# Optimization experiments

Measured on AMD Instinct MI355X. Metric: run time of the kernel, lower is better.

## Reference

```python
import jax, jax.numpy as jnp
import numpy as np

NMS_RADIUS = 0.05  # matches init_kwargs nms_radius


def setup_inputs() -> dict:
    key = jax.random.key(0)
    heatmap = jax.random.normal(key, (64, 1, 1024, 1024), dtype=jnp.float32)
    return {"heatmap": heatmap, "num_candidates": 16}


def _nms_select(coords, num_keep, radius):
    """Greedy sequential 2D NMS over score-sorted coords [k,2].
    torch.topk already returns values sorted descending, so the torch
    argsort(descending=True) is the identity permutation here."""
    k = coords.shape[0]
    # pairwise euclidean distances [k,k]
    d = jnp.linalg.norm(coords[:, None, :] - coords[None, :, :], axis=-1)

    def body(carry, i):
        mask, count = carry  # mask[j] = candidate j already selected
        too_close = jnp.any((d[i] < radius) & mask)
        accept = jnp.logical_and(~too_close, count < num_keep)
        mask = mask.at[i].set(accept)
        count = count + accept.astype(jnp.int32)
        return (mask, count), None

    (mask, _), _ = jax.lax.scan(body, (jnp.zeros(k, bool), jnp.int32(0)), jnp.arange(k))
    # compact: place selected coords (in score order) into the first num_keep slots
    pos = jnp.cumsum(mask) - 1               # output slot for each selected candidate
    slot = jnp.where(mask, pos, num_keep)    # out-of-range slot for unselected -> dropped
    out = jnp.zeros((num_keep, 2), coords.dtype).at[slot].set(coords, mode="drop")
    return out


def reference(heatmap, num_candidates):
    B, _, H, W = heatmap.shape
    flat = heatmap.reshape(B, H * W)
    k = min(num_candidates * 4, H * W)
    top_vals, top_idx = jax.lax.top_k(flat, k)   # sorted descending, like torch.topk
    ty = top_idx // W
    tx = top_idx % W
    # normalized (x, y) in [0,1], shape [B, k, 2]
    coords = jnp.stack([tx.astype(jnp.float32) / (W - 1),
                        ty.astype(jnp.float32) / (H - 1)], axis=-1)
    return jax.vmap(lambda c: _nms_select(c, num_candidates, NMS_RADIUS))(coords)
```

## Files before the change

### kernel.cpp

```cpp
#include <hip/hip_runtime.h>
#include <float.h>
#include <limits.h>

#define RADIUS 0.05f
#define TH     3.0f
#define LCAP   1024
#define SORTN  2048

typedef unsigned long long u64;

__device__ __forceinline__ unsigned fkey(float f) {
  unsigned u = __float_as_uint(f);
  return (u & 0x80000000u) ? ~u : (u | 0x80000000u);
}

__global__ __launch_bounds__(256) void zero_k(unsigned* cnt, int* bad, int B) {
  int t = blockIdx.x * blockDim.x + threadIdx.x;
  if (t < B * 16) cnt[t] = 0u;
  if (t < B) bad[t] = 0;
}

__global__ __launch_bounds__(256) void scan_collect(
    const float* __restrict__ hm, unsigned* __restrict__ cnt, int* __restrict__ bad,
    u64* __restrict__ buf, int bcap, int elems, int chunk) {
  const int b   = blockIdx.y;
  const int tid = threadIdx.x;
  const int vbase = blockIdx.x * chunk;
  const float4* p = (const float4*)(hm + (size_t)b * elems) + vbase;

  __shared__ u64 sbuf[LCAP];
  __shared__ unsigned sh, sbase;
  if (tid == 0) sh = 0u;
  __syncthreads();

  auto push = [&](float v, int idx) {
    if (v > TH) {
      unsigned pos = atomicAdd(&sh, 1u);
      if (pos < LCAP)
        sbuf[pos] = ((u64)(__float_as_uint(v) | 0x80000000u) << 32) | (unsigned)(~idx);
    }
  };

  int chunkMain = chunk & ~1023;
  for (int i = tid; i < chunkMain; i += 1024) {
    float4 v0 = p[i], v1 = p[i + 256], v2 = p[i + 512], v3 = p[i + 768];
    int g0 = (vbase + i) << 2, g1 = (vbase + i + 256) << 2;
    int g2 = (vbase + i + 512) << 2, g3 = (vbase + i + 768) << 2;
    push(v0.x, g0); push(v0.y, g0 + 1); push(v0.z, g0 + 2); push(v0.w, g0 + 3);
    push(v1.x, g1); push(v1.y, g1 + 1); push(v1.z, g1 + 2); push(v1.w, g1 + 3);
    push(v2.x, g2); push(v2.y, g2 + 1); push(v2.z, g2 + 2); push(v2.w, g2 + 3);
    push(v3.x, g3); push(v3.y, g3 + 1); push(v3.z, g3 + 2); push(v3.w, g3 + 3);
  }
  for (int i = chunkMain + tid; i < chunk; i += 256) {
    float4 v = p[i];
    int g = (vbase + i) << 2;
    push(v.x, g); push(v.y, g + 1); push(v.z, g + 2); push(v.w, g + 3);
  }

  __syncthreads();
  unsigned h = sh;
  unsigned stored = h < (unsigned)LCAP ? h : (unsigned)LCAP;
  if (tid == 0) {
    sbase = atomicAdd(&cnt[b * 16], stored);
    if (h > (unsigned)LCAP || sbase + stored > (unsigned)bcap) atomicExch(&bad[b], 1);
  }
  __syncthreads();
  unsigned gb = sbase;
  for (unsigned i = tid; i < stored; i += 256) {
    unsigned dst = gb + i;
    if (dst < (unsigned)bcap) buf[(size_t)b * bcap + dst] = sbuf[i];
  }
}

__global__ __launch_bounds__(256) void select_k(
    const float* __restrict__ hm, const unsigned* __restrict__ cnt,
    const int* __restrict__ bad, const u64* __restrict__ buf, int bcap,
    float* __restrict__ out, int W, int H, int K, int nk, int elems) {
  const int b = blockIdx.x, tid = threadIdx.x;

  __shared__ u64 s[SORTN];
  __shared__ unsigned s_cnt;
  __shared__ int s_m;
  __shared__ float topx[64], topy[64];
  __shared__ float outbuf[128];

  int c = 0;
  bool good = false;
  if (bcap > 0) {
    c = (int)cnt[b * 16];
    good = (!bad[b]) && (c >= K) && (c <= bcap) && (c <= SORTN);
  }

  if (good) {
    for (int i = tid; i < SORTN; i += 256)
      s[i] = (i < c) ? buf[(size_t)b * bcap + i] : 0ull;
  } else {
    unsigned lo = 0u, hi = 0xFFFFFFFFu;
    const float4* p4 = (const float4*)(hm + (size_t)b * elems);
    const int nvec4 = elems >> 2;
    while (lo < hi) {
      unsigned mid = lo + ((hi - lo) >> 1) + 1u;
      if (tid == 0) s_cnt = 0u;
      __syncthreads();
      unsigned local = 0;
      for (int i = tid; i < nvec4; i += 256) {
        float4 v = p4[i];
        local += (fkey(v.x) >= mid) + (fkey(v.y) >= mid) + (fkey(v.z) >= mid) + (fkey(v.w) >= mid);
      }
      atomicAdd(&s_cnt, local);
      __syncthreads();
      if (s_cnt >= (unsigned)K) lo = mid; else hi = mid - 1u;
      __syncthreads();
    }
    if (tid == 0) s_m = 0;
    __syncthreads();
    const float* q = hm + (size_t)b * elems;
    for (int i = tid; i < elems; i += 256) {
      unsigned kk = fkey(q[i]);
      if (kk >= lo) {
        int pos = atomicAdd(&s_m, 1);
        if (pos < SORTN) s[pos] = ((u64)kk << 32) | (unsigned)(~i);
      }
    }
    __syncthreads();
    int c2 = s_m < SORTN ? s_m : SORTN;
    for (int i = tid; i < SORTN; i += 256)
      if (i >= c2) s[i] = 0ull;
  }
  __syncthreads();

  for (int k2 = 2; k2 <= SORTN; k2 <<= 1) {
    for (int j = k2 >> 1; j > 0; j >>= 1) {
      for (int i = tid; i < SORTN; i += 256) {
        int ix = i ^ j;
        if (ix > i) {
          u64 a = s[i], bb = s[ix];
          bool desc = ((i & k2) == 0);
          bool sw = desc ? (a < bb) : (a > bb);
          if (sw) { s[i] = bb; s[ix] = a; }
        }
      }
      __syncthreads();
    }
  }

  const float invW = 1.0f / (float)(W - 1);
  const float invH = 1.0f / (float)(H - 1);
  if (tid < K) {
    u64 e = s[tid];
    int idx = (int)(~(unsigned)(e & 0xFFFFFFFFu));
    int ty = idx / W;
    int tx = idx - ty * W;
    topx[tid] = (float)tx * invW;
    topy[tid] = (float)ty * invH;
  }
  for (int i = tid; i < 2 * nk; i += 256) outbuf[i] = 0.0f;
  __syncthreads();

  if (tid < 64) {
    float myx = (tid < K) ? topx[tid] : 0.0f;
    float myy = (tid < K) ? topy[tid] : 0.0f;
    bool sel = false;
    int cntA = 0;
    for (int i = 0; i < K; i++) {
      float xi = __shfl(myx, i);
      float yi = __shfl(myy, i);
      float dx = myx - xi, dy = myy - yi;
      bool close = sel && (sqrtf(dx * dx + dy * dy) < RADIUS);
      u64 anym = __ballot(close);
      bool accept = (anym == 0ull) && (cntA < nk);
      if (tid == i) sel = accept;
      cntA += accept ? 1 : 0;
    }
    u64 selball = __ballot(sel);
    if (sel) {
      int slot = __popcll(selball & ((1ull << tid) - 1ull));
      if (slot < nk) { outbuf[2 * slot] = myx; outbuf[2 * slot + 1] = myy; }
    }
  }
  __syncthreads();

  float* outp = out + (size_t)b * 2 * nk;
  for (int i = tid; i < 2 * nk; i += 256) outp[i] = outbuf[i];
}

extern "C" void kernel_launch(void* const* d_in, const int* in_sizes, int n_in,
                              void* d_out, int out_size, void* d_ws, size_t ws_size,
                              hipStream_t stream) {
  const float* hm = (const float*)d_in[0];
  const int H = 1024, W = 1024;
  const int elems = H * W;
  int B = in_sizes[0] / elems;
  int nk = out_size / (B * 2);
  int K = 4 * nk;
  if (K > elems) K = elems;
  if (K > 64) K = 64;

  unsigned* cnt = (unsigned*)d_ws;
  size_t off_bad = (size_t)B * 16 * sizeof(unsigned);
  int* bad = (int*)((char*)d_ws + off_bad);
  size_t off_buf = (off_bad + (size_t)B * sizeof(int) + 255) & ~(size_t)255;
  u64* buf = (u64*)((char*)d_ws + off_buf);
  int bcap = 0;
  if (ws_size > off_buf) {
    size_t avail = ws_size - off_buf;
    long long capl = (long long)(avail / ((size_t)B * sizeof(u64)));
    bcap = (capl > SORTN) ? SORTN : (int)capl;
  }

  zero_k<<<(B * 16 + 255) / 256, 256, 0, stream>>>(cnt, bad, B);
  if (bcap > 0) {
    const int gx = 16;
    int chunk = (elems >> 2) / gx;
    dim3 grid(gx, B);
    scan_collect<<<grid, 256, 0, stream>>>(hm, cnt, bad, buf, bcap, elems, chunk);
  }
  select_k<<<B, 256, 0, stream>>>(hm, cnt, bad, buf, bcap, (float*)d_out, W, H, K, nk, elems);
}
```

Baseline: 440.3 us.

## Replace full 2048-element bitonic sort with radix-select threshold and small top sort

Each scan block now writes its candidates to a private per-block segment with its own count, which removes the zero kernel, the global atomic counter and the bad flag. The select kernel concatenates the segments, binary-searches a key threshold over the candidates in shared memory to isolate the top K, and then bitonic-sorts only 128 entries instead of 2048. Wave-level shuffle reductions replace per-thread shared atomics in the counting loops. This cuts the sorting work and one kernel launch, but the per-block buffer shrinks to 256 entries, so overflow forces the slow full-heatmap fallback more often.

```diff
diff --git a/kernel.cpp b/kernel.cpp
--- a/kernel.cpp
+++ b/kernel.cpp
@@ -1,11 +1,10 @@
 #include <hip/hip_runtime.h>
-#include <float.h>
-#include <limits.h>
 
 #define RADIUS 0.05f
 #define TH     3.0f
-#define LCAP   1024
+#define SBUF   256
 #define SORTN  2048
+#define TOPC   128
 
 typedef unsigned long long u64;
 
@@ -14,29 +13,24 @@
   return (u & 0x80000000u) ? ~u : (u | 0x80000000u);
 }
 
-__global__ __launch_bounds__(256) void zero_k(unsigned* cnt, int* bad, int B) {
-  int t = blockIdx.x * blockDim.x + threadIdx.x;
-  if (t < B * 16) cnt[t] = 0u;
-  if (t < B) bad[t] = 0;
-}
-
 __global__ __launch_bounds__(256) void scan_collect(
-    const float* __restrict__ hm, unsigned* __restrict__ cnt, int* __restrict__ bad,
-    u64* __restrict__ buf, int bcap, int elems, int chunk) {
+    const float* __restrict__ hm, unsigned* __restrict__ cnt,
+    u64* __restrict__ buf, int bcapblk, int elems, int chunk) {
   const int b   = blockIdx.y;
+  const int g   = blockIdx.x;
   const int tid = threadIdx.x;
-  const int vbase = blockIdx.x * chunk;
+  const int vbase = g * chunk;
   const float4* p = (const float4*)(hm + (size_t)b * elems) + vbase;
 
-  __shared__ u64 sbuf[LCAP];
-  __shared__ unsigned sh, sbase;
+  __shared__ u64 sbuf[SBUF];
+  __shared__ unsigned sh;
   if (tid == 0) sh = 0u;
   __syncthreads();
 
   auto push = [&](float v, int idx) {
     if (v > TH) {
       unsigned pos = atomicAdd(&sh, 1u);
-      if (pos < LCAP)
+      if (pos < SBUF)
         sbuf[pos] = ((u64)(__float_as_uint(v) | 0x80000000u) << 32) | (unsigned)(~idx);
     }
   };
@@ -53,47 +47,87 @@
   }
   for (int i = chunkMain + tid; i < chunk; i += 256) {
     float4 v = p[i];
-    int g = (vbase + i) << 2;
-    push(v.x, g); push(v.y, g + 1); push(v.z, g + 2); push(v.w, g + 3);
+    int gg = (vbase + i) << 2;
+    push(v.x, gg); push(v.y, gg + 1); push(v.z, gg + 2); push(v.w, gg + 3);
   }
 
   __syncthreads();
   unsigned h = sh;
-  unsigned stored = h < (unsigned)LCAP ? h : (unsigned)LCAP;
-  if (tid == 0) {
-    sbase = atomicAdd(&cnt[b * 16], stored);
-    if (h > (unsigned)LCAP || sbase + stored > (unsigned)bcap) atomicExch(&bad[b], 1);
-  }
-  __syncthreads();
-  unsigned gb = sbase;
-  for (unsigned i = tid; i < stored; i += 256) {
-    unsigned dst = gb + i;
-    if (dst < (unsigned)bcap) buf[(size_t)b * bcap + dst] = sbuf[i];
-  }
+  unsigned cap = (unsigned)bcapblk; if (cap > (unsigned)SBUF) cap = SBUF;
+  unsigned stored = h < cap ? h : cap;
+  u64* dst = buf + (size_t)(b * 16 + g) * (size_t)bcapblk;
+  for (unsigned i = tid; i < stored; i += 256) dst[i] = sbuf[i];
+  if (tid == 0)
+    cnt[b * 16 + g] = stored | (h > stored ? 0x80000000u : 0u);
 }
 
 __global__ __launch_bounds__(256) void select_k(
     const float* __restrict__ hm, const unsigned* __restrict__ cnt,
-    const int* __restrict__ bad, const u64* __restrict__ buf, int bcap,
+    const u64* __restrict__ buf, int bcapblk,
     float* __restrict__ out, int W, int H, int K, int nk, int elems) {
   const int b = blockIdx.x, tid = threadIdx.x;
 
   __shared__ u64 s[SORTN];
+  __shared__ unsigned skey[SORTN];
+  __shared__ u64 top[TOPC];
+  __shared__ unsigned segoff[17];
+  __shared__ int s_good, s_m;
   __shared__ unsigned s_cnt;
-  __shared__ int s_m;
   __shared__ float topx[64], topy[64];
   __shared__ float outbuf[128];
 
-  int c = 0;
-  bool good = false;
-  if (bcap > 0) {
-    c = (int)cnt[b * 16];
-    good = (!bad[b]) && (c >= K) && (c <= bcap) && (c <= SORTN);
-  }
+  if (tid == 0) {
+    unsigned tot = 0; int ok = (bcapblk > 0);
+    for (int g = 0; g < 16; g++) {
+      unsigned cv = (bcapblk > 0) ? cnt[b * 16 + g] : 0u;
+      segoff[g] = tot;
+      if (cv & 0x80000000u) ok = 0;
+      tot += (cv & 0x7FFFFFFFu);
+    }
+    segoff[16] = tot;
+    s_good = ok && tot >= (unsigned)K && tot <= (unsigned)SORTN;
+    s_m = 0;
+  }
+  __syncthreads();
+  const int good = s_good;
+  const unsigned c = segoff[16];
 
   if (good) {
-    for (int i = tid; i < SORTN; i += 256)
-      s[i] = (i < c) ? buf[(size_t)b * bcap + i] : 0ull;
+    for (int g = 0; g < 16; g++) {
+      unsigned off = segoff[g], len = segoff[g + 1] - off;
+      const u64* src = buf + (size_t)(b * 16 + g) * (size_t)bcapblk;
+      for (unsigned i = tid; i < len; i += 256) {
+        u64 e = src[i];
+        s[off + i] = e;
+        skey[off + i] = (unsigned)(e >> 32);
+      }
+    }
+    __syncthreads();
+
+    unsigned lo = 0xC0400000u;
+    unsigned hi = 0xFFFFFFFFu;
+    while (lo < hi) {
+      unsigned mid = lo + ((hi - lo) >> 1) + 1u;
+      if (tid == 0) s_cnt = 0u;
+      __syncthreads();
+      unsigned local = 0;
+      for (unsigned i = tid; i < c; i += 256) local += (skey[i] >= mid);
+      #pragma unroll
+      for (int o = 32; o > 0; o >>= 1) local += __shfl_xor(local, o);
+      if ((tid & 63) == 0) atomicAdd(&s_cnt, local);
+      __syncthreads();
+      unsigned tot = s_cnt;
+      if (tot >= (unsigned)K) lo = mid; else hi = mid - 1u;
+      __syncthreads();
+    }
+
+    for (unsigned i = tid; i < c; i += 256) {
+      if (skey[i] >= lo) {
+        int p = atomicAdd(&s_m, 1);
+        if (p < TOPC) top[p] = s[i];
+      }
+    }
+    __syncthreads();
   } else {
     unsigned lo = 0u, hi = 0xFFFFFFFFu;
     const float4* p4 = (const float4*)(hm + (size_t)b * elems);
@@ -107,37 +141,35 @@
         float4 v = p4[i];
         local += (fkey(v.x) >= mid) + (fkey(v.y) >= mid) + (fkey(v.z) >= mid) + (fkey(v.w) >= mid);
       }
-      atomicAdd(&s_cnt, local);
+      #pragma unroll
+      for (int o = 32; o > 0; o >>= 1) local += __shfl_xor(local, o);
+      if ((tid & 63) == 0) atomicAdd(&s_cnt, local);
       __syncthreads();
       if (s_cnt >= (unsigned)K) lo = mid; else hi = mid - 1u;
       __syncthreads();
     }
-    if (tid == 0) s_m = 0;
-    __syncthreads();
     const float* q = hm + (size_t)b * elems;
     for (int i = tid; i < elems; i += 256) {
       unsigned kk = fkey(q[i]);
       if (kk >= lo) {
-        int pos = atomicAdd(&s_m, 1);
-        if (pos < SORTN) s[pos] = ((u64)kk << 32) | (unsigned)(~i);
+        int p = atomicAdd(&s_m, 1);
+        if (p < TOPC) top[p] = ((u64)kk << 32) | (unsigned)(~i);
       }
     }
     __syncthreads();
-    int c2 = s_m < SORTN ? s_m : SORTN;
-    for (int i = tid; i < SORTN; i += 256)
-      if (i >= c2) s[i] = 0ull;
-  }
-  __syncthreads();
-
-  for (int k2 = 2; k2 <= SORTN; k2 <<= 1) {
+  }
+
+  int m = s_m; if (m > TOPC) m = TOPC;
+  for (int i = tid; i < TOPC; i += 256) if (i >= m) top[i] = 0ull;
+  __syncthreads();
+  for (int k2 = 2; k2 <= TOPC; k2 <<= 1) {
     for (int j = k2 >> 1; j > 0; j >>= 1) {
-      for (int i = tid; i < SORTN; i += 256) {
-        int ix = i ^ j;
-        if (ix > i) {
-          u64 a = s[i], bb = s[ix];
-          bool desc = ((i & k2) == 0);
-          bool sw = desc ? (a < bb) : (a > bb);
-          if (sw) { s[i] = bb; s[ix] = a; }
+      if (tid < TOPC) {
+        int ix = tid ^ j;
+        if (ix > tid) {
+          u64 a = top[tid], bb = top[ix];
+          bool desc = ((tid & k2) == 0);
+          if (desc ? (a < bb) : (a > bb)) { top[tid] = bb; top[ix] = a; }
         }
       }
       __syncthreads();
@@ -147,7 +179,7 @@
   const float invW = 1.0f / (float)(W - 1);
   const float invH = 1.0f / (float)(H - 1);
   if (tid < K) {
-    u64 e = s[tid];
+    u64 e = top[tid];
     int idx = (int)(~(unsigned)(e & 0xFFFFFFFFu));
     int ty = idx / W;
     int tx = idx - ty * W;
@@ -197,23 +229,21 @@
   if (K > 64) K = 64;
 
   unsigned* cnt = (unsigned*)d_ws;
-  size_t off_bad = (size_t)B * 16 * sizeof(unsigned);
-  int* bad = (int*)((char*)d_ws + off_bad);
-  size_t off_buf = (off_bad + (size_t)B * sizeof(int) + 255) & ~(size_t)255;
+  size_t off_buf = ((size_t)B * 16 * sizeof(unsigned) + 255) & ~(size_t)255;
   u64* buf = (u64*)((char*)d_ws + off_buf);
-  int bcap = 0;
+  int bcapblk = 0;
   if (ws_size > off_buf) {
     size_t avail = ws_size - off_buf;
-    long long capl = (long long)(avail / ((size_t)B * sizeof(u64)));
-    bcap = (capl > SORTN) ? SORTN : (int)capl;
-  }
-
-  zero_k<<<(B * 16 + 255) / 256, 256, 0, stream>>>(cnt, bad, B);
-  if (bcap > 0) {
+    long long capl = (long long)(avail / ((size_t)B * 16 * sizeof(u64)));
+    bcapblk = (capl > SBUF) ? SBUF : (int)capl;
+    if (bcapblk < 16) bcapblk = 0;
+  }
+
+  if (bcapblk > 0) {
     const int gx = 16;
     int chunk = (elems >> 2) / gx;
     dim3 grid(gx, B);
-    scan_collect<<<grid, 256, 0, stream>>>(hm, cnt, bad, buf, bcap, elems, chunk);
-  }
-  select_k<<<B, 256, 0, stream>>>(hm, cnt, bad, buf, bcap, (float*)d_out, W, H, K, nk, elems);
-}
+    scan_collect<<<grid, 256, 0, stream>>>(hm, cnt, buf, bcapblk, elems, chunk);
+  }
+  select_k<<<B, 256, 0, stream>>>(hm, cnt, buf, bcapblk, (float*)d_out, W, H, K, nk, elems);
+}
```

After: 400.3 us. 1.1x faster.
